# Performance work log

Hardware: AMD Instinct MI355X
Metric: run time of the kernel (lower is better)

Reference implementation:

```python
import jax, jax.numpy as jnp
import numpy as np

FORWARD_STEPS = 300


def setup_inputs() -> dict:
    key = jax.random.key(0)
    k1, k2, k3, k4 = jax.random.split(key, 4)
    B, T, F = 1024, 2048, 16
    return {
        "vi": jax.random.uniform(k1, (B,), dtype=jnp.float32),
        "delta_y": jax.random.uniform(k2, (B,), dtype=jnp.float32),
        "v_previous": jax.random.uniform(k3, (B,), dtype=jnp.float32),
        "x_input": jax.random.uniform(k4, (B, T, F), dtype=jnp.float32),
        "w": jnp.asarray(4.1, dtype=jnp.float32),  # learned scalar, init Constant(4.1)
    }


def _newell_forward(x_input, w, forward_steps):
    B, T, F = x_input.shape
    x_last = x_input[:, -1, :]                     # [B, F]
    i_idx = jnp.arange(forward_steps, dtype=jnp.float32)  # [S]

    temps, valids = [], []
    for j in (1, 2, 3, 4):  # unrolled while_loop body, j=1..4
        d = jnp.sum(x_last[:, :j], axis=-1)        # [B]
        td = d * 150.0 / (w + x_last[:, 4 + j] * 25.0)  # [B]
        # referred_index = cast(i - td*10, int32) then clip to [0, T-1]
        ref = (i_idx[:, None] - (td * 10.0)[None, :]).astype(jnp.int32)  # [S, B]
        ref = jnp.clip(ref, 0, T - 1)
        feat = x_input[:, :, 9 + j]                # [B, T]
        temp = jnp.take_along_axis(feat, ref.T, axis=1).T  # [S, B]
        temps.append(temp)
        valids.append(jnp.any(temp != 0, axis=1))  # [S] — reduce_any over batch

    temps = jnp.stack(temps, axis=1)               # [S, 4, B]
    valid = jnp.stack(valids, axis=1)              # [S, 4]
    # early-exit semantics: ahat = temp of FIRST j with any nonzero, else zeros
    sel = jnp.argmax(valid, axis=1)                # [S]
    ahat = jnp.take_along_axis(temps, sel[:, None, None], axis=1)[:, 0, :]  # [S, B]
    ahat = jnp.where(jnp.any(valid, axis=1)[:, None], ahat, jnp.float32(0.0))
    return ahat.T                                  # [B, S] == stack(predictions, axis=1)


def reference(vi, delta_y, v_previous, x_input, w):
    return _newell_forward(x_input, w, FORWARD_STEPS)
```

## Files before the change

kernel.cpp:

```cpp
#include <hip/hip_runtime.h>

#define T_DIM 2048
#define F_DIM 16
#define B_DIM 1024
#define STEPS 300
#define TC 304

#define OFF_CBUF  (4u * B_DIM * TC * 4u)
#define OFF_NZ    (OFF_CBUF + 4u * B_DIM * 4u)
#define OFF_VALID (OFF_NZ + 4u * B_DIM * 5u * 8u)

__global__ void __launch_bounds__(320) kA(const float* __restrict__ x,
                                          const float* __restrict__ wptr,
                                          float* __restrict__ F,
                                          float* __restrict__ cbuf,
                                          unsigned long long* __restrict__ NZ,
                                          unsigned long long* __restrict__ validw) {
#pragma clang fp contract(off)
    int b = blockIdx.x;
    int t = threadIdx.x;
    if (b == 0 && t < 20) validw[t] = 0ull;

    if (t == 0) {
        const float* xl = x + ((size_t)b * T_DIM + (T_DIM - 1)) * F_DIM;
        float w = *wptr;
        float d = 0.0f;
#pragma unroll
        for (int j0 = 0; j0 < 4; ++j0) {
            d = d + xl[j0];
            float den = w + xl[5 + j0] * 25.0f;
            float td  = (d * 150.0f) / den;
            cbuf[j0 * B_DIM + b] = td * 10.0f;
        }
    }

    float v0 = 0.f, v1 = 0.f, v2 = 0.f, v3 = 0.f;
    bool act = t < STEPS;
    if (act) {
        const float* row = x + ((size_t)b * T_DIM + t) * F_DIM;
        float2 p0 = *(const float2*)(row + 10);
        float2 p1 = *(const float2*)(row + 12);
        v0 = p0.x; v1 = p0.y; v2 = p1.x; v3 = p1.y;
        F[((size_t)(0 * B_DIM + b)) * TC + t] = v0;
        F[((size_t)(1 * B_DIM + b)) * TC + t] = v1;
        F[((size_t)(2 * B_DIM + b)) * TC + t] = v2;
        F[((size_t)(3 * B_DIM + b)) * TC + t] = v3;
    }
    unsigned long long m0 = __ballot(act && v0 != 0.f);
    unsigned long long m1 = __ballot(act && v1 != 0.f);
    unsigned long long m2 = __ballot(act && v2 != 0.f);
    unsigned long long m3 = __ballot(act && v3 != 0.f);
    int w = t >> 6;
    if ((t & 63) == 0) {
        NZ[((size_t)(0 * B_DIM + b)) * 5 + w] = m0;
        NZ[((size_t)(1 * B_DIM + b)) * 5 + w] = m1;
        NZ[((size_t)(2 * B_DIM + b)) * 5 + w] = m2;
        NZ[((size_t)(3 * B_DIM + b)) * 5 + w] = m3;
    }
}

__global__ void __launch_bounds__(256) kB(const float* __restrict__ cbuf,
                                          const unsigned long long* __restrict__ NZ,
                                          unsigned long long* __restrict__ validw) {
#pragma clang fp contract(off)
    int tid = blockIdx.x * 256 + threadIdx.x;
    int b  = tid & 1023;
    int wj = tid >> 10;
    int j  = wj & 3;
    int w  = wj >> 2;
    float c = cbuf[j * B_DIM + b];
    const unsigned long long* nzp = NZ + (size_t)(j * B_DIM + b) * 5;
    unsigned long long nz0 = nzp[0], nz1 = nzp[1], nz2 = nzp[2], nz3 = nzp[3], nz4 = nzp[4];

    unsigned long long a = 0;
    int kmax = (w == 4) ? (STEPS - 256) : 64;
    for (int k = 0; k < kmax; ++k) {
        int i = w * 64 + k;
        float r = (float)i - c;
        int idx = (int)r;
        idx = idx < 0 ? 0 : (idx > STEPS - 1 ? STEPS - 1 : idx);
        unsigned long long word = idx < 64 ? nz0 : idx < 128 ? nz1 :
                                  idx < 192 ? nz2 : idx < 256 ? nz3 : nz4;
        a |= ((word >> (idx & 63)) & 1ull) << k;
    }
    unsigned lo = (unsigned)a, hi = (unsigned)(a >> 32);
#pragma unroll
    for (int s = 32; s; s >>= 1) {
        lo |= __shfl_xor(lo, s, 64);
        hi |= __shfl_xor(hi, s, 64);
    }
    if ((threadIdx.x & 63) == 0) {
        unsigned long long red = ((unsigned long long)hi << 32) | lo;
        if (red) atomicOr(&validw[j * 5 + w], red);
    }
}

__global__ void __launch_bounds__(256) kC(const float* __restrict__ F,
                                          const float* __restrict__ cbuf,
                                          const unsigned long long* __restrict__ validw,
                                          float* __restrict__ out) {
#pragma clang fp contract(off)
    int g = blockIdx.x * 256 + threadIdx.x;
    if (g >= B_DIM * STEPS) return;
    int b = g / STEPS;
    int i = g - b * STEPS;
    int wi = i >> 6, bi = i & 63;
    unsigned m = 0;
#pragma unroll
    for (int j = 0; j < 4; ++j)
        m |= (unsigned)((validw[j * 5 + wi] >> bi) & 1ull) << j;
    float r = 0.0f;
    if (m) {
        int j = __ffs(m) - 1;
        float c = cbuf[j * B_DIM + b];
        float rr = (float)i - c;
        int idx = (int)rr;
        idx = idx < 0 ? 0 : (idx > STEPS - 1 ? STEPS - 1 : idx);
        r = F[(size_t)(j * B_DIM + b) * TC + idx];
    }
    out[g] = r;
}

extern "C" void kernel_launch(void* const* d_in, const int* in_sizes, int n_in,
                              void* d_out, int out_size, void* d_ws, size_t ws_size,
                              hipStream_t stream) {
    const float* x    = (const float*)d_in[3];
    const float* wptr = (const float*)d_in[4];
    float* out = (float*)d_out;

    float*              Fbuf   = (float*)d_ws;
    float*              cbuf   = (float*)((char*)d_ws + OFF_CBUF);
    unsigned long long* NZ     = (unsigned long long*)((char*)d_ws + OFF_NZ);
    unsigned long long* validw = (unsigned long long*)((char*)d_ws + OFF_VALID);

    hipLaunchKernelGGL(kA, dim3(B_DIM), dim3(320), 0, stream, x, wptr, Fbuf, cbuf, NZ, validw);
    hipLaunchKernelGGL(kB, dim3(80), dim3(256), 0, stream, cbuf, NZ, validw);
    hipLaunchKernelGGL(kC, dim3((B_DIM * STEPS + 255) / 256), dim3(256), 0, stream,
                       Fbuf, cbuf, validw, out);
}
```

Measured before the change: 186.7 us.

## Fuse validity computation into first kernel using shared memory, drop F/NZ buffers

Kernel A now handles four batch rows per block, stages the four feature columns in shared memory, evaluates the gathered nonzero test directly, and ORs per-wave ballots into the global valid words with atomics. The separate bitmask kernel and the NZ and F workspace buffers go away. Kernel C now gathers straight from the input tensor instead of the compacted F buffer. This removes one launch and the workspace write/read traffic, at the cost of strided gathers from x in kC, a memset launch, and more atomics.

Measured after the change: 206.1 us. 1.1x slower.

```diff
diff --git a/kernel.cpp b/kernel.cpp
--- a/kernel.cpp
+++ b/kernel.cpp
@@ -4,98 +4,67 @@
 #define F_DIM 16
 #define B_DIM 1024
 #define STEPS 300
-#define TC 304
+#define BPB 4
 
-#define OFF_CBUF  (4u * B_DIM * TC * 4u)
-#define OFF_NZ    (OFF_CBUF + 4u * B_DIM * 4u)
-#define OFF_VALID (OFF_NZ + 4u * B_DIM * 5u * 8u)
+#define OFF_VALID 16384u
 
 __global__ void __launch_bounds__(320) kA(const float* __restrict__ x,
                                           const float* __restrict__ wptr,
-                                          float* __restrict__ F,
                                           float* __restrict__ cbuf,
-                                          unsigned long long* __restrict__ NZ,
                                           unsigned long long* __restrict__ validw) {
 #pragma clang fp contract(off)
-    int b = blockIdx.x;
+    __shared__ float sF[4][STEPS];
+    __shared__ float sc[4];
     int t = threadIdx.x;
-    if (b == 0 && t < 20) validw[t] = 0ull;
+    int wv = t >> 6;
+    unsigned long long acc[4] = {0ull, 0ull, 0ull, 0ull};
 
-    if (t == 0) {
-        const float* xl = x + ((size_t)b * T_DIM + (T_DIM - 1)) * F_DIM;
-        float w = *wptr;
-        float d = 0.0f;
 #pragma unroll
-        for (int j0 = 0; j0 < 4; ++j0) {
-            d = d + xl[j0];
-            float den = w + xl[5 + j0] * 25.0f;
-            float td  = (d * 150.0f) / den;
-            cbuf[j0 * B_DIM + b] = td * 10.0f;
+    for (int s = 0; s < BPB; ++s) {
+        int b = blockIdx.x * BPB + s;
+        if (t == 0) {
+            const float* xl = x + ((size_t)b * T_DIM + (T_DIM - 1)) * F_DIM;
+            float w = *wptr;
+            float d = 0.0f;
+#pragma unroll
+            for (int j0 = 0; j0 < 4; ++j0) {
+                d = d + xl[j0];
+                float den = w + xl[5 + j0] * 25.0f;
+                float td  = (d * 150.0f) / den;
+                float c   = td * 10.0f;
+                sc[j0] = c;
+                cbuf[j0 * B_DIM + b] = c;
+            }
         }
+        if (t < STEPS) {
+            const float* row = x + ((size_t)b * T_DIM + t) * F_DIM;
+            float2 p0 = *(const float2*)(row + 10);
+            float2 p1 = *(const float2*)(row + 12);
+            sF[0][t] = p0.x; sF[1][t] = p0.y; sF[2][t] = p1.x; sF[3][t] = p1.y;
+        }
+        __syncthreads();
+        bool act = t < STEPS;
+#pragma unroll
+        for (int j = 0; j < 4; ++j) {
+            bool bit = false;
+            if (act) {
+                float r = (float)t - sc[j];
+                int idx = (int)r;
+                idx = idx < 0 ? 0 : (idx > STEPS - 1 ? STEPS - 1 : idx);
+                bit = sF[j][idx] != 0.0f;
+            }
+            acc[j] |= __ballot(bit);
+        }
+        __syncthreads();
     }
-
-    float v0 = 0.f, v1 = 0.f, v2 = 0.f, v3 = 0.f;
-    bool act = t < STEPS;
-    if (act) {
-        const float* row = x + ((size_t)b * T_DIM + t) * F_DIM;
-        float2 p0 = *(const float2*)(row + 10);
-        float2 p1 = *(const float2*)(row + 12);
-        v0 = p0.x; v1 = p0.y; v2 = p1.x; v3 = p1.y;
-        F[((size_t)(0 * B_DIM + b)) * TC + t] = v0;
-        F[((size_t)(1 * B_DIM + b)) * TC + t] = v1;
-        F[((size_t)(2 * B_DIM + b)) * TC + t] = v2;
-        F[((size_t)(3 * B_DIM + b)) * TC + t] = v3;
-    }
-    unsigned long long m0 = __ballot(act && v0 != 0.f);
-    unsigned long long m1 = __ballot(act && v1 != 0.f);
-    unsigned long long m2 = __ballot(act && v2 != 0.f);
-    unsigned long long m3 = __ballot(act && v3 != 0.f);
-    int w = t >> 6;
     if ((t & 63) == 0) {
-        NZ[((size_t)(0 * B_DIM + b)) * 5 + w] = m0;
-        NZ[((size_t)(1 * B_DIM + b)) * 5 + w] = m1;
-        NZ[((size_t)(2 * B_DIM + b)) * 5 + w] = m2;
-        NZ[((size_t)(3 * B_DIM + b)) * 5 + w] = m3;
+#pragma unroll
+        for (int j = 0; j < 4; ++j)
+            if (acc[j]) atomicOr(&validw[j * 5 + wv], acc[j]);
     }
 }
 
-__global__ void __launch_bounds__(256) kB(const float* __restrict__ cbuf,
-                                          const unsigned long long* __restrict__ NZ,
-                                          unsigned long long* __restrict__ validw) {
-#pragma clang fp contract(off)
-    int tid = blockIdx.x * 256 + threadIdx.x;
-    int b  = tid & 1023;
-    int wj = tid >> 10;
-    int j  = wj & 3;
-    int w  = wj >> 2;
-    float c = cbuf[j * B_DIM + b];
-    const unsigned long long* nzp = NZ + (size_t)(j * B_DIM + b) * 5;
-    unsigned long long nz0 = nzp[0], nz1 = nzp[1], nz2 = nzp[2], nz3 = nzp[3], nz4 = nzp[4];
-
-    unsigned long long a = 0;
-    int kmax = (w == 4) ? (STEPS - 256) : 64;
-    for (int k = 0; k < kmax; ++k) {
-        int i = w * 64 + k;
-        float r = (float)i - c;
-        int idx = (int)r;
-        idx = idx < 0 ? 0 : (idx > STEPS - 1 ? STEPS - 1 : idx);
-        unsigned long long word = idx < 64 ? nz0 : idx < 128 ? nz1 :
-                                  idx < 192 ? nz2 : idx < 256 ? nz3 : nz4;
-        a |= ((word >> (idx & 63)) & 1ull) << k;
-    }
-    unsigned lo = (unsigned)a, hi = (unsigned)(a >> 32);
-#pragma unroll
-    for (int s = 32; s; s >>= 1) {
-        lo |= __shfl_xor(lo, s, 64);
-        hi |= __shfl_xor(hi, s, 64);
-    }
-    if ((threadIdx.x & 63) == 0) {
-        unsigned long long red = ((unsigned long long)hi << 32) | lo;
-        if (red) atomicOr(&validw[j * 5 + w], red);
-    }
-}
-
-__global__ void __launch_bounds__(256) kC(const float* __restrict__ F,
+__global__ void __launch_bounds__(256) kC(const float* __restrict__ x,
                                           const float* __restrict__ cbuf,
                                           const unsigned long long* __restrict__ validw,
                                           float* __restrict__ out) {
@@ -116,7 +85,7 @@
         float rr = (float)i - c;
         int idx = (int)rr;
         idx = idx < 0 ? 0 : (idx > STEPS - 1 ? STEPS - 1 : idx);
-        r = F[(size_t)(j * B_DIM + b) * TC + idx];
+        r = x[((size_t)b * T_DIM + idx) * F_DIM + 10 + j];
     }
     out[g] = r;
 }
@@ -128,13 +97,11 @@
     const float* wptr = (const float*)d_in[4];
     float* out = (float*)d_out;
 
-    float*              Fbuf   = (float*)d_ws;
-    float*              cbuf   = (float*)((char*)d_ws + OFF_CBUF);
-    unsigned long long* NZ     = (unsigned long long*)((char*)d_ws + OFF_NZ);
+    float*              cbuf   = (float*)d_ws;
     unsigned long long* validw = (unsigned long long*)((char*)d_ws + OFF_VALID);
 
-    hipLaunchKernelGGL(kA, dim3(B_DIM), dim3(320), 0, stream, x, wptr, Fbuf, cbuf, NZ, validw);
-    hipLaunchKernelGGL(kB, dim3(80), dim3(256), 0, stream, cbuf, NZ, validw);
+    hipMemsetAsync(validw, 0, 20 * sizeof(unsigned long long), stream);
+    hipLaunchKernelGGL(kA, dim3(B_DIM / BPB), dim3(320), 0, stream, x, wptr, cbuf, validw);
     hipLaunchKernelGGL(kC, dim3((B_DIM * STEPS + 255) / 256), dim3(256), 0, stream,
-                       Fbuf, cbuf, validw, out);
+                       x, cbuf, validw, out);
 }
```
